# Kernel optimization log

Hardware: AMD Instinct MI355X
Metric: run time of the kernel (lower is better)

Reference implementation:

```python
import jax, jax.numpy as jnp
import numpy as np


def setup_inputs() -> dict:
    key = jax.random.key(0)
    k1, k2, k3, k4 = jax.random.split(key, 4)
    B, G, C, T = 4, 40, 13, 1024
    return {
        "x": jax.random.normal(k1, (B, G, C, T), dtype=jnp.float32),
        "query_w": jax.random.normal(k2, (C, C), dtype=jnp.float32),
        "key_w": jax.random.normal(k3, (C, C), dtype=jnp.float32),
        "value_w": jax.random.normal(k4, (C, C), dtype=jnp.float32),
    }


def reference(x, query_w, key_w, value_w):
    # x: [B, 40, 13, T] real -> rfft over time -> [B, 40, 13, F] complex
    x_fft = jnp.fft.rfft(x, axis=-1)
    cdt = x_fft.dtype
    wq = query_w.astype(cdt)  # [13,13] complex (zero imag), shared across the 40 groups
    wk = key_w.astype(cdt)
    wv = value_w.astype(cdt)
    xt = jnp.swapaxes(x_fft, -1, -2)  # [B, 40, F, 13]
    q = xt @ wq                       # [B, 40, F, 13]
    k = xt @ wk
    v = xt @ wv
    scores = jnp.abs(q @ jnp.swapaxes(k, -1, -2))     # [B, 40, F, F] real
    attn = jax.nn.softmax(scores, axis=-1).astype(cdt)
    out = (attn @ v)                                   # [B, 40, F, 13]
    out = jnp.swapaxes(out, -1, -2)                    # [B, 40, 13, F]
    return jnp.fft.irfft(out, axis=-1)                 # [B, 40, 13, 2*(F-1)]
```

## Files before the change

kernel.cpp:

```cpp
#include <hip/hip_runtime.h>
#include <math.h>

#define BDIM 4
#define GDIM 40
#define CDIM 13
#define TDIM 1024
#define FDIM 513
#define BG   (BDIM*GDIM)
#define NROW (BG*FDIM)
#define NCHUNK 9
#define TK 64
#define QW 64

typedef _Float16 half4 __attribute__((ext_vector_type(4)));
typedef _Float16 half8 __attribute__((ext_vector_type(8)));
typedef float    f32x4 __attribute__((ext_vector_type(4)));

#define MFMA16(a, b, c) __builtin_amdgcn_mfma_f32_16x16x16f16((a), (b), (c), 0, 0, 0)

__device__ __forceinline__ unsigned bitrev10(unsigned x) { return __brev(x) >> 22; }

__global__ void fft_fwd2(const float* __restrict__ x, float2* __restrict__ xf) {
    __shared__ float re[1024], im[1024];
    const int s2 = blockIdx.x;
    const float* x1 = x + (size_t)(2 * s2) * TDIM;
    const float* x2 = x1 + TDIM;
    for (int t = threadIdx.x; t < 1024; t += blockDim.x) {
        unsigned r = bitrev10(t);
        re[r] = x1[t];
        im[r] = x2[t];
    }
    __syncthreads();
    for (int s = 0; s < 10; ++s) {
        int half = 1 << s;
        for (int j = threadIdx.x; j < 512; j += blockDim.x) {
            int grp = j >> s;
            int pos = j & (half - 1);
            int i1 = (grp << (s + 1)) + pos;
            int i2 = i1 + half;
            float ang = -(float)M_PI * (float)pos / (float)half;
            float sw, cw; __sincosf(ang, &sw, &cw);
            float xr = re[i2], xi = im[i2];
            float tr = cw * xr - sw * xi;
            float ti = cw * xi + sw * xr;
            float ur = re[i1], ui = im[i1];
            re[i1] = ur + tr; im[i1] = ui + ti;
            re[i2] = ur - tr; im[i2] = ui - ti;
        }
        __syncthreads();
    }
    const int sigA = 2 * s2, sigB = sigA + 1;
    const int bgA = sigA / CDIM, cA = sigA % CDIM;
    const int bgB = sigB / CDIM, cB = sigB % CDIM;
    for (int f = threadIdx.x; f < FDIM; f += blockDim.x) {
        int fr = (1024 - f) & 1023;
        float zr = re[f], zi = im[f];
        float wr = re[fr], wi = im[fr];
        xf[((size_t)bgA * FDIM + f) * CDIM + cA] =
            make_float2(0.5f * (zr + wr), 0.5f * (zi - wi));
        xf[((size_t)bgB * FDIM + f) * CDIM + cB] =
            make_float2(0.5f * (zi + wi), 0.5f * (wr - zr));
    }
}

__global__ __launch_bounds__(256) void qkv_kernel(const float2* __restrict__ xf,
                           const float* __restrict__ wq,
                           const float* __restrict__ wk,
                           const float* __restrict__ wv,
                           float2* __restrict__ q,
                           _Float16* __restrict__ KP,
                           _Float16* __restrict__ VT) {
    __shared__ float2   Xs[QW * CDIM];
    __shared__ float    Ws[3 * CDIM * CDIM];
    __shared__ _Float16 KPs[QW * 72];
    __shared__ _Float16 VTs[32 * 72];

    const int bg    = blockIdx.x / NCHUNK;
    const int ch    = blockIdx.x % NCHUNK;
    const int f0    = ch * QW;
    const int nrows = min(QW, FDIM - f0);
    const int tid   = threadIdx.x;
    const int nitems = nrows * CDIM;

    for (int idx = tid; idx < nitems; idx += 256)
        Xs[idx] = xf[((size_t)bg * FDIM + f0) * CDIM + idx];
    for (int idx = tid; idx < 3 * 169; idx += 256)
        Ws[idx] = (idx < 169) ? wq[idx] : ((idx < 338) ? wk[idx - 169] : wv[idx - 338]);
    for (int z = tid; z < 6 * QW; z += 256) {
        int rr = z >> 6, jj = z & 63;
        int pc = (rr < 3) ? (13 + rr) : (29 + (rr - 3));
        VTs[pc * 72 + jj] = (_Float16)0.f;
    }
    __syncthreads();

    for (int item = tid; item < nitems; item += 256) {
        int row = item / CDIM;
        int i   = item - row * CDIM;
        const float2* xrow = &Xs[row * CDIM];
        float qr = 0, qi = 0, kr = 0, ki = 0, vr = 0, vi = 0;
#pragma unroll
        for (int c = 0; c < CDIM; ++c) {
            float2 xc = xrow[c];
            float a = Ws[c * CDIM + i];       qr += xc.x * a; qi += xc.y * a;
            float b = Ws[169 + c * CDIM + i]; kr += xc.x * b; ki += xc.y * b;
            float d = Ws[338 + c * CDIM + i]; vr += xc.x * d; vi += xc.y * d;
        }
        q[((size_t)bg * FDIM + f0) * CDIM + item] = make_float2(qr, qi);
        _Float16* kp = KPs + row * 72;
        _Float16 h0 = (_Float16)kr, h1 = (_Float16)ki;
        kp[i]      = h0;
        kp[13 + i] = h1;
        kp[32 + i] = (_Float16)(kr - (float)h0);
        kp[45 + i] = (_Float16)(ki - (float)h1);
        if (i == 12) {
            *(unsigned*)(kp + 26) = 0u; *(unsigned*)(kp + 28) = 0u; *(unsigned*)(kp + 30) = 0u;
            *(unsigned*)(kp + 58) = 0u; *(unsigned*)(kp + 60) = 0u; *(unsigned*)(kp + 62) = 0u;
        }
        VTs[i * 72 + row]        = (_Float16)vr;
        VTs[(16 + i) * 72 + row] = (_Float16)vi;
    }
    __syncthreads();

    _Float16* KPg = KP + ((size_t)bg * FDIM + f0) * 64;
    _Float16* VTg = VT + (size_t)bg * 2 * 16 * 520 + f0;
    if (nrows == QW) {
        for (int idx = tid; idx < QW * 8; idx += 256) {
            int row = idx >> 3, gg = idx & 7;
            *(half8*)(KPg + row * 64 + gg * 8) = *(const half8*)(KPs + row * 72 + gg * 8);
        }
        for (int idx = tid; idx < 32 * 8; idx += 256) {
            int pc = idx >> 3, j8 = idx & 7;
            *(half8*)(VTg + pc * 520 + j8 * 8) = *(const half8*)(VTs + pc * 72 + j8 * 8);
        }
    } else {
        for (int idx = tid; idx < nrows * 8; idx += 256) {
            int row = idx >> 3, gg = idx & 7;
            *(half8*)(KPg + row * 64 + gg * 8) = *(const half8*)(KPs + row * 72 + gg * 8);
        }
        if (tid < 32) VTg[tid * 520] = VTs[tid * 72];
    }
}

__global__ __launch_bounds__(256, 4) void attn_kernel(const float2* __restrict__ q,
                                                      const _Float16* __restrict__ KP,
                                                      const _Float16* __restrict__ VT,
                                                      float2* __restrict__ outspec) {
    __shared__ __align__(16) _Float16 Klds[TK * 64];
    __shared__ __align__(16) _Float16 VTlds[2 * 16 * 72];

    const int bg    = blockIdx.x / NCHUNK;
    const int chunk = blockIdx.x % NCHUNK;
    const int tid   = threadIdx.x;
    const int w     = tid >> 6;
    const int lane  = tid & 63;
    const int qlane = lane & 15;
    const int g     = lane >> 4;
    const int frow  = chunk * 64 + w * 16 + qlane;
    const bool writer = (frow < FDIM);
    const int f     = writer ? frow : (FDIM - 1);
    const size_t rowbase = ((size_t)bg * FDIM + f) * CDIM;

    half4 uh[2], ul[2], u2h[2], u2l[2];
#pragma unroll
    for (int c01 = 0; c01 < 2; ++c01) {
#pragma unroll
        for (int j = 0; j < 4; ++j) {
            int k = c01 * 16 + 4 * g + j;
            float a = 0.f, b = 0.f;
            if (k < CDIM) {
                float2 t = q[rowbase + k];          a = t.x;  b = t.y;
            } else if (k < 2 * CDIM) {
                float2 t = q[rowbase + (k - CDIM)]; a = -t.y; b = t.x;
            }
            _Float16 ah = (_Float16)a;
            uh[c01][j]  = ah;
            ul[c01][j]  = (_Float16)(a - (float)ah);
            _Float16 bh = (_Float16)b;
            u2h[c01][j] = bh;
            u2l[c01][j] = (_Float16)(b - (float)bh);
        }
    }

    f32x4 o_re = {0.f, 0.f, 0.f, 0.f};
    f32x4 o_im = {0.f, 0.f, 0.f, 0.f};
    float m = -INFINITY, l = 0.f;

    const _Float16* __restrict__ KPg = KP + (size_t)bg * FDIM * 64;
    const _Float16* __restrict__ VTg = VT + (size_t)bg * 2 * 16 * 520;

    for (int t0 = 0; t0 < FDIM; t0 += TK) {
        __syncthreads();
#pragma unroll
        for (int hh = 0; hh < 2; ++hh) {
            int gr  = tid + hh * 256;
            int krw = gr >> 3, gg = gr & 7;
            half8 val;
#pragma unroll
            for (int e = 0; e < 8; ++e) val[e] = (_Float16)0.f;
            int grow = t0 + krw;
            if (grow < FDIM)
                val = *(const half8*)(KPg + (size_t)grow * 64 + gg * 8);
            *(half8*)(Klds + krw * 64 + ((gg ^ (krw & 7)) << 3)) = val;
        }
        {
            int gk = tid & 7, cc = (tid >> 3) & 15, part = tid >> 7;
            int rb = t0 + gk * 8;
            half8 val;
#pragma unroll
            for (int e = 0; e < 8; ++e) val[e] = (_Float16)0.f;
            if (rb < FDIM) {
                val = *(const half8*)(VTg + ((size_t)(part * 16 + cc)) * 520 + rb);
                if (rb + 8 > FDIM) {
#pragma unroll
                    for (int e = 0; e < 8; ++e) if (rb + e >= FDIM) val[e] = (_Float16)0.f;
                }
            }
            *(half8*)(VTlds + (part * 16 + cc) * 72 + gk * 8) = val;
        }
        __syncthreads();

#pragma unroll
        for (int sub = 0; sub < 4; ++sub) {
            const int arow = sub * 16 + qlane;
            const int rx   = arow & 7;
            const _Float16* kr = Klds + arow * 64;
#define KFRAG(h) (*(const half4*)(kr + (((((h) >> 3)) ^ rx) << 3) + ((h) & 7)))
            half4 wh0 = KFRAG(4 * g);
            half4 wh1 = KFRAG(16 + 4 * g);
            half4 wl0 = KFRAG(32 + 4 * g);
            half4 wl1 = KFRAG(48 + 4 * g);
#undef KFRAG
            f32x4 sre = {0.f, 0.f, 0.f, 0.f};
            f32x4 sim = {0.f, 0.f, 0.f, 0.f};
            sre = MFMA16(wh0, uh[0], sre);
            sre = MFMA16(wh1, uh[1], sre);
            sre = MFMA16(wl0, uh[0], sre);
            sre = MFMA16(wl1, uh[1], sre);
            sre = MFMA16(wh0, ul[0], sre);
            sre = MFMA16(wh1, ul[1], sre);
            sre = MFMA16(wl0, ul[0], sre);
            sre = MFMA16(wl1, ul[1], sre);
            sim = MFMA16(wh0, u2h[0], sim);
            sim = MFMA16(wh1, u2h[1], sim);
            sim = MFMA16(wl0, u2h[0], sim);
            sim = MFMA16(wl1, u2h[1], sim);
            sim = MFMA16(wh0, u2l[0], sim);
            sim = MFMA16(wh1, u2l[1], sim);
            sim = MFMA16(wl0, u2l[0], sim);
            sim = MFMA16(wl1, u2l[1], sim);

            float s0 = sqrtf(fmaf(sre[0], sre[0], sim[0] * sim[0]));
            float s1 = sqrtf(fmaf(sre[1], sre[1], sim[1] * sim[1]));
            float s2 = sqrtf(fmaf(sre[2], sre[2], sim[2] * sim[2]));
            float s3 = sqrtf(fmaf(sre[3], sre[3], sim[3] * sim[3]));
            float tmax = fmaxf(fmaxf(s0, s1), fmaxf(s2, s3));
            tmax = fmaxf(tmax, __shfl_xor(tmax, 16));
            tmax = fmaxf(tmax, __shfl_xor(tmax, 32));
            float mnew  = fmaxf(m, tmax);
            float alpha = __expf(m - mnew);
            m = mnew;
            l *= alpha;
            o_re *= alpha;
            o_im *= alpha;
            float p0 = __expf(s0 - m);
            float p1 = __expf(s1 - m);
            float p2 = __expf(s2 - m);
            float p3 = __expf(s3 - m);
            l += (p0 + p1) + (p2 + p3);
            half4 pk;
            pk[0] = (_Float16)p0; pk[1] = (_Float16)p1;
            pk[2] = (_Float16)p2; pk[3] = (_Float16)p3;

            const int voff = sub * 16 + 4 * g;
            half4 vfr = *(const half4*)(VTlds + qlane * 72 + voff);
            half4 vfi = *(const half4*)(VTlds + (16 + qlane) * 72 + voff);
            o_re = MFMA16(vfr, pk, o_re);
            o_im = MFMA16(vfi, pk, o_im);
        }
    }

    l += __shfl_xor(l, 16);
    l += __shfl_xor(l, 32);
    if (writer) {
        float inv = 1.f / l;
#pragma unroll
        for (int j = 0; j < 4; ++j) {
            int c = 4 * g + j;
            if (c < CDIM)
                outspec[((size_t)(bg * CDIM + c)) * FDIM + frow] =
                    make_float2(o_re[j] * inv, o_im[j] * inv);
        }
    }
}

__global__ void fft_inv2(const float2* __restrict__ spec, float* __restrict__ out) {
    __shared__ float re[1024], im[1024];
    const int s2 = blockIdx.x;
    const float2* Y1 = spec + (size_t)(2 * s2) * FDIM;
    const float2* Y2 = Y1 + FDIM;
    for (int t = threadIdx.x; t < 1024; t += blockDim.x) {
        float a, b, c, d;
        if (t <= 512) {
            float2 y1 = Y1[t], y2 = Y2[t];
            bool edge = (t == 0) | (t == 512);
            a = y1.x; b = edge ? 0.f : y1.y;
            c = y2.x; d = edge ? 0.f : y2.y;
        } else {
            float2 y1 = Y1[1024 - t], y2 = Y2[1024 - t];
            a = y1.x; b = -y1.y;
            c = y2.x; d = -y2.y;
        }
        unsigned r = bitrev10(t);
        re[r] = a - d;
        im[r] = b + c;
    }
    __syncthreads();
    for (int s = 0; s < 10; ++s) {
        int half = 1 << s;
        for (int j = threadIdx.x; j < 512; j += blockDim.x) {
            int grp = j >> s;
            int pos = j & (half - 1);
            int i1 = (grp << (s + 1)) + pos;
            int i2 = i1 + half;
            float ang = (float)M_PI * (float)pos / (float)half;
            float sw, cw; __sincosf(ang, &sw, &cw);
            float xr = re[i2], xi = im[i2];
            float tr = cw * xr - sw * xi;
            float ti = cw * xi + sw * xr;
            float ur = re[i1], ui = im[i1];
            re[i1] = ur + tr; im[i1] = ui + ti;
            re[i2] = ur - tr; im[i2] = ui - ti;
        }
        __syncthreads();
    }
    const float scale = 1.0f / 1024.0f;
    float* o1 = out + (size_t)(2 * s2) * TDIM;
    for (int t = threadIdx.x; t < 1024; t += blockDim.x) {
        o1[t]        = re[t] * scale;
        o1[TDIM + t] = im[t] * scale;
    }
}

extern "C" void kernel_launch(void* const* d_in, const int* in_sizes, int n_in,
                              void* d_out, int out_size, void* d_ws, size_t ws_size,
                              hipStream_t stream) {
    const float* x  = (const float*)d_in[0];
    const float* wq = (const float*)d_in[1];
    const float* wk = (const float*)d_in[2];
    const float* wv = (const float*)d_in[3];
    float* out = (float*)d_out;

    const size_t n = (size_t)NROW * CDIM;
    float2* xf = (float2*)d_ws;
    float2* q  = xf + n;
    _Float16* KP = (_Float16*)(q + n);
    _Float16* VT = KP + (size_t)NROW * 64;

    fft_fwd2<<<BG * CDIM / 2, 512, 0, stream>>>(x, xf);
    qkv_kernel<<<BG * NCHUNK, 256, 0, stream>>>(xf, wq, wk, wv, q, KP, VT);
    attn_kernel<<<BG * NCHUNK, 256, 0, stream>>>(q, KP, VT, xf );
    fft_inv2<<<BG * CDIM / 2, 512, 0, stream>>>(xf, out);
}
```

Baseline: 178.9 us.

## Fuse forward FFT and QKV projection into one kernel per batch-group

Merges the forward real FFT and the QKV projection into a single kernel with one 512-thread block per (batch, group). The full 13x513 spectrum stays in shared memory, which removes the global xf round trip and one launch. The cost is that only 160 blocks run, each with about 63 KB of LDS and 7 sequential FFT passes, so parallelism is much lower than the previous 1040 FFT blocks plus 1440 QKV blocks.

```diff
diff --git a/kernel.cpp b/kernel.cpp
--- a/kernel.cpp
+++ b/kernel.cpp
@@ -10,7 +10,7 @@
 #define NROW (BG*FDIM)
 #define NCHUNK 9
 #define TK 64
-#define QW 64
+#define QW2 32
 
 typedef _Float16 half4 __attribute__((ext_vector_type(4)));
 typedef _Float16 half8 __attribute__((ext_vector_type(8)));
@@ -20,124 +20,123 @@
 
 __device__ __forceinline__ unsigned bitrev10(unsigned x) { return __brev(x) >> 22; }
 
-__global__ void fft_fwd2(const float* __restrict__ x, float2* __restrict__ xf) {
-    __shared__ float re[1024], im[1024];
-    const int s2 = blockIdx.x;
-    const float* x1 = x + (size_t)(2 * s2) * TDIM;
-    const float* x2 = x1 + TDIM;
-    for (int t = threadIdx.x; t < 1024; t += blockDim.x) {
-        unsigned r = bitrev10(t);
-        re[r] = x1[t];
-        im[r] = x2[t];
+__global__ __launch_bounds__(512) void fwdqkv_kernel(
+    const float* __restrict__ x,
+    const float* __restrict__ wq, const float* __restrict__ wk,
+    const float* __restrict__ wv,
+    float2* __restrict__ q, _Float16* __restrict__ KP, _Float16* __restrict__ VT)
+{
+    __shared__ __align__(16) char smem[63600];
+    float2*   Xs  = (float2*)smem;
+    float*    Ws  = (float*)(smem + 53360);
+    float*    re  = (float*)(smem + 55408);
+    float*    im  = re + 1024;
+    _Float16* KPs = (_Float16*)(smem + 55408);
+    _Float16* VTs = KPs + 32 * 72;
+
+    const int bg  = blockIdx.x;
+    const int tid = threadIdx.x;
+
+    if (tid < 507)
+        Ws[tid] = (tid < 169) ? wq[tid] : ((tid < 338) ? wk[tid - 169] : wv[tid - 338]);
+
+    for (int pr = 0; pr < 7; ++pr) {
+        const int cA = 2 * pr, cB = 2 * pr + 1;
+        const bool hasB = (cB < CDIM);
+        const float* x1 = x + ((size_t)bg * CDIM + cA) * TDIM;
+        const float* x2 = x + ((size_t)bg * CDIM + (hasB ? cB : cA)) * TDIM;
+        __syncthreads();
+        for (int t = tid; t < 1024; t += 512) {
+            unsigned r = bitrev10(t);
+            re[r] = x1[t];
+            im[r] = hasB ? x2[t] : 0.f;
+        }
+        __syncthreads();
+        for (int s = 0; s < 10; ++s) {
+            int half = 1 << s;
+            {
+                int j = tid;
+                int grp = j >> s;
+                int pos = j & (half - 1);
+                int i1 = (grp << (s + 1)) + pos;
+                int i2 = i1 + half;
+                float ang = -(float)M_PI * (float)pos / (float)half;
+                float sw, cw; __sincosf(ang, &sw, &cw);
+                float xr = re[i2], xi = im[i2];
+                float tr = cw * xr - sw * xi;
+                float ti = cw * xi + sw * xr;
+                float ur = re[i1], ui = im[i1];
+                re[i1] = ur + tr; im[i1] = ui + ti;
+                re[i2] = ur - tr; im[i2] = ui - ti;
+            }
+            __syncthreads();
+        }
+        for (int f = tid; f < FDIM; f += 512) {
+            int fr = (1024 - f) & 1023;
+            float zr = re[f], zi = im[f];
+            float wr = re[fr], wi = im[fr];
+            Xs[cA * FDIM + f] = make_float2(0.5f * (zr + wr), 0.5f * (zi - wi));
+            if (hasB)
+                Xs[cB * FDIM + f] = make_float2(0.5f * (zi + wi), 0.5f * (wr - zr));
+        }
     }
     __syncthreads();
-    for (int s = 0; s < 10; ++s) {
-        int half = 1 << s;
-        for (int j = threadIdx.x; j < 512; j += blockDim.x) {
-            int grp = j >> s;
-            int pos = j & (half - 1);
-            int i1 = (grp << (s + 1)) + pos;
-            int i2 = i1 + half;
-            float ang = -(float)M_PI * (float)pos / (float)half;
-            float sw, cw; __sincosf(ang, &sw, &cw);
-            float xr = re[i2], xi = im[i2];
-            float tr = cw * xr - sw * xi;
-            float ti = cw * xi + sw * xr;
-            float ur = re[i1], ui = im[i1];
-            re[i1] = ur + tr; im[i1] = ui + ti;
-            re[i2] = ur - tr; im[i2] = ui - ti;
-        }
-        __syncthreads();
-    }
-    const int sigA = 2 * s2, sigB = sigA + 1;
-    const int bgA = sigA / CDIM, cA = sigA % CDIM;
-    const int bgB = sigB / CDIM, cB = sigB % CDIM;
-    for (int f = threadIdx.x; f < FDIM; f += blockDim.x) {
-        int fr = (1024 - f) & 1023;
-        float zr = re[f], zi = im[f];
-        float wr = re[fr], wi = im[fr];
-        xf[((size_t)bgA * FDIM + f) * CDIM + cA] =
-            make_float2(0.5f * (zr + wr), 0.5f * (zi - wi));
-        xf[((size_t)bgB * FDIM + f) * CDIM + cB] =
-            make_float2(0.5f * (zi + wi), 0.5f * (wr - zr));
-    }
-}
-
-__global__ __launch_bounds__(256) void qkv_kernel(const float2* __restrict__ xf,
-                           const float* __restrict__ wq,
-                           const float* __restrict__ wk,
-                           const float* __restrict__ wv,
-                           float2* __restrict__ q,
-                           _Float16* __restrict__ KP,
-                           _Float16* __restrict__ VT) {
-    __shared__ float2   Xs[QW * CDIM];
-    __shared__ float    Ws[3 * CDIM * CDIM];
-    __shared__ _Float16 KPs[QW * 72];
-    __shared__ _Float16 VTs[32 * 72];
-
-    const int bg    = blockIdx.x / NCHUNK;
-    const int ch    = blockIdx.x % NCHUNK;
-    const int f0    = ch * QW;
-    const int nrows = min(QW, FDIM - f0);
-    const int tid   = threadIdx.x;
-    const int nitems = nrows * CDIM;
-
-    for (int idx = tid; idx < nitems; idx += 256)
-        Xs[idx] = xf[((size_t)bg * FDIM + f0) * CDIM + idx];
-    for (int idx = tid; idx < 3 * 169; idx += 256)
-        Ws[idx] = (idx < 169) ? wq[idx] : ((idx < 338) ? wk[idx - 169] : wv[idx - 338]);
-    for (int z = tid; z < 6 * QW; z += 256) {
-        int rr = z >> 6, jj = z & 63;
+
+    if (tid < 6 * QW2) {
+        int rr = tid >> 5, jj = tid & 31;
         int pc = (rr < 3) ? (13 + rr) : (29 + (rr - 3));
-        VTs[pc * 72 + jj] = (_Float16)0.f;
-    }
-    __syncthreads();
-
-    for (int item = tid; item < nitems; item += 256) {
-        int row = item / CDIM;
-        int i   = item - row * CDIM;
-        const float2* xrow = &Xs[row * CDIM];
-        float qr = 0, qi = 0, kr = 0, ki = 0, vr = 0, vi = 0;
-#pragma unroll
-        for (int c = 0; c < CDIM; ++c) {
-            float2 xc = xrow[c];
-            float a = Ws[c * CDIM + i];       qr += xc.x * a; qi += xc.y * a;
-            float b = Ws[169 + c * CDIM + i]; kr += xc.x * b; ki += xc.y * b;
-            float d = Ws[338 + c * CDIM + i]; vr += xc.x * d; vi += xc.y * d;
-        }
-        q[((size_t)bg * FDIM + f0) * CDIM + item] = make_float2(qr, qi);
-        _Float16* kp = KPs + row * 72;
-        _Float16 h0 = (_Float16)kr, h1 = (_Float16)ki;
-        kp[i]      = h0;
-        kp[13 + i] = h1;
-        kp[32 + i] = (_Float16)(kr - (float)h0);
-        kp[45 + i] = (_Float16)(ki - (float)h1);
-        if (i == 12) {
-            *(unsigned*)(kp + 26) = 0u; *(unsigned*)(kp + 28) = 0u; *(unsigned*)(kp + 30) = 0u;
-            *(unsigned*)(kp + 58) = 0u; *(unsigned*)(kp + 60) = 0u; *(unsigned*)(kp + 62) = 0u;
-        }
-        VTs[i * 72 + row]        = (_Float16)vr;
-        VTs[(16 + i) * 72 + row] = (_Float16)vi;
-    }
-    __syncthreads();
-
-    _Float16* KPg = KP + ((size_t)bg * FDIM + f0) * 64;
-    _Float16* VTg = VT + (size_t)bg * 2 * 16 * 520 + f0;
-    if (nrows == QW) {
-        for (int idx = tid; idx < QW * 8; idx += 256) {
-            int row = idx >> 3, gg = idx & 7;
-            *(half8*)(KPg + row * 64 + gg * 8) = *(const half8*)(KPs + row * 72 + gg * 8);
-        }
-        for (int idx = tid; idx < 32 * 8; idx += 256) {
-            int pc = idx >> 3, j8 = idx & 7;
-            *(half8*)(VTg + pc * 520 + j8 * 8) = *(const half8*)(VTs + pc * 72 + j8 * 8);
-        }
-    } else {
-        for (int idx = tid; idx < nrows * 8; idx += 256) {
-            int row = idx >> 3, gg = idx & 7;
-            *(half8*)(KPg + row * 64 + gg * 8) = *(const half8*)(KPs + row * 72 + gg * 8);
-        }
-        if (tid < 32) VTg[tid * 520] = VTs[tid * 72];
+        VTs[pc * 40 + jj] = (_Float16)0.f;
+    }
+
+    for (int ch = 0; ch < 17; ++ch) {
+        const int f0 = ch * QW2;
+        const int nrows = min(QW2, FDIM - f0);
+        const int nitems = nrows * CDIM;
+        __syncthreads();
+        for (int item = tid; item < nitems; item += 512) {
+            int row = item / CDIM;
+            int i   = item - row * CDIM;
+            int f   = f0 + row;
+            float qr = 0, qi = 0, kr = 0, ki = 0, vr = 0, vi = 0;
+#pragma unroll
+            for (int c = 0; c < CDIM; ++c) {
+                float2 xc = Xs[c * FDIM + f];
+                float a = Ws[c * CDIM + i];       qr += xc.x * a; qi += xc.y * a;
+                float b = Ws[169 + c * CDIM + i]; kr += xc.x * b; ki += xc.y * b;
+                float d = Ws[338 + c * CDIM + i]; vr += xc.x * d; vi += xc.y * d;
+            }
+            q[((size_t)bg * FDIM + f) * CDIM + i] = make_float2(qr, qi);
+            _Float16* kp = KPs + row * 72;
+            _Float16 h0 = (_Float16)kr, h1 = (_Float16)ki;
+            kp[i]      = h0;
+            kp[13 + i] = h1;
+            kp[32 + i] = (_Float16)(kr - (float)h0);
+            kp[45 + i] = (_Float16)(ki - (float)h1);
+            if (i == 12) {
+                *(unsigned*)(kp + 26) = 0u; *(unsigned*)(kp + 28) = 0u; *(unsigned*)(kp + 30) = 0u;
+                *(unsigned*)(kp + 58) = 0u; *(unsigned*)(kp + 60) = 0u; *(unsigned*)(kp + 62) = 0u;
+            }
+            VTs[i * 40 + row]        = (_Float16)vr;
+            VTs[(16 + i) * 40 + row] = (_Float16)vi;
+        }
+        __syncthreads();
+        _Float16* KPg = KP + ((size_t)bg * FDIM + f0) * 64;
+        _Float16* VTg = VT + (size_t)bg * 2 * 16 * 520 + f0;
+        if (nrows == QW2) {
+            if (tid < QW2 * 8) {
+                int row = tid >> 3, gg = tid & 7;
+                *(half8*)(KPg + row * 64 + gg * 8) = *(const half8*)(KPs + row * 72 + gg * 8);
+            } else if (tid < QW2 * 8 + 32 * 4) {
+                int t2 = tid - QW2 * 8;
+                int pc = t2 >> 2, j8 = t2 & 3;
+                *(half8*)(VTg + pc * 520 + j8 * 8) = *(const half8*)(VTs + pc * 40 + j8 * 8);
+            }
+        } else {
+            if (tid < 8)
+                *(half8*)(KPg + tid * 8) = *(const half8*)(KPs + tid * 8);
+            else if (tid >= 32 && tid < 64)
+                VTg[(tid - 32) * 520] = VTs[(tid - 32) * 40];
+        }
     }
 }
 
@@ -351,13 +350,12 @@
     float* out = (float*)d_out;
 
     const size_t n = (size_t)NROW * CDIM;
-    float2* xf = (float2*)d_ws;
-    float2* q  = xf + n;
+    float2* outspec = (float2*)d_ws;
+    float2* q  = outspec + n;
     _Float16* KP = (_Float16*)(q + n);
     _Float16* VT = KP + (size_t)NROW * 64;
 
-    fft_fwd2<<<BG * CDIM / 2, 512, 0, stream>>>(x, xf);
-    qkv_kernel<<<BG * NCHUNK, 256, 0, stream>>>(xf, wq, wk, wv, q, KP, VT);
-    attn_kernel<<<BG * NCHUNK, 256, 0, stream>>>(q, KP, VT, xf );
-    fft_inv2<<<BG * CDIM / 2, 512, 0, stream>>>(xf, out);
+    fwdqkv_kernel<<<BG, 512, 0, stream>>>(x, wq, wk, wv, q, KP, VT);
+    attn_kernel<<<BG * NCHUNK, 256, 0, stream>>>(q, KP, VT, outspec);
+    fft_inv2<<<BG * CDIM / 2, 512, 0, stream>>>(outspec, out);
 }
```

Result: slower. 186.4 us (+4.2%).
